# Optimization experiments

Hardware: AMD Instinct MI355X
Metric: run time of the kernel (lower is better)

Reference implementation:

```python
import jax, jax.numpy as jnp
import numpy as np

H = 1024            # hinges
S = 4               # shims
N = H + 2           # nodes
NC = 2 * N          # flattened DOFs
B = 256             # batch of independent chains
L = 1.0             # rest edge length
DT = 0.001          # integration step
GAMMA = 2.0         # damping
N_STEPS = 64        # relaxation steps (truncated scan)


def setup_inputs() -> dict:
    key = jax.random.key(0)
    k1, k2, k3, k4, k5 = jax.random.split(key, 5)
    xs = jnp.arange(N, dtype=jnp.float32) * L
    base = jnp.stack([xs, jnp.zeros(N, jnp.float32)], axis=-1)          # (N,2) straight chain
    noise = 0.01 * jax.random.normal(k1, (B, N, 2), jnp.float32)
    noise = noise.at[:, :2, :].set(0.0)                                  # nodes 0,1 fixed exactly
    pos0 = base[None] + noise                                            # (B,N,2)
    tip_base = base[-1]
    tip_off = jnp.stack([-0.1 * L * H * jax.random.uniform(k2, (B,)),
                         2.0 * jax.random.normal(k3, (B,))], axis=-1)
    tip_pos = (tip_base[None] + tip_off).astype(jnp.float32)             # (B,2) imposed tip
    thetas_ss = 0.3 * jax.random.uniform(k4, (H,), jnp.float32)          # snap-through angles
    buckle_arr = jax.random.randint(k5, (H, S), 0, 2).astype(jnp.int32)  # {0,1} -> maps to {-1,+1}
    return dict(pos0=pos0, tip_pos=tip_pos, thetas_ss=thetas_ss, buckle_arr=buckle_arr,
                k_stiff=jnp.float32(10.0), k_soft=jnp.float32(0.5), k_stretch=jnp.float32(1000.0))


def _free_mask():
    m = np.ones(NC, bool)
    m[:4] = False            # nodes 0,1 fixed (dof_idx = 2*node+comp)
    m[2 * (N - 1):] = False  # tip node imposed
    return jnp.asarray(m)


def _energy(x, thetas_ss, buckle_pm, k_stiff, k_soft, k_stretch):
    """Total potential energy of one chain; x is flattened (NC,)."""
    pos = x.reshape(N, 2)
    v1 = pos[1:-1] - pos[:-2]                 # (H,2) edge into hinge h
    v2 = pos[2:] - pos[1:-1]                  # (H,2) edge out of hinge h
    theta = jnp.arctan2(v1[:, 0] * v2[:, 1] - v1[:, 1] * v2[:, 0],
                        jnp.sum(v1 * v2, -1))               # (H,) CCW hinge angle
    d = pos[1:] - pos[:-1]
    elen = jnp.sqrt(jnp.sum(d * d, -1))                     # (H+1,) edge lengths
    T = theta[:, None]                                      # (H,1)
    TH = thetas_ss[:, None]                                 # (H,1)
    stiff = ((buckle_pm == 1) & (T < TH)) | ((buckle_pm == -1) & (T > -TH))  # (H,S)
    k_rot = jnp.where(stiff, k_stiff, k_soft)
    e_rot = 0.5 * jnp.sum(k_rot * (T - TH) ** 2)
    e_str = 0.5 * jnp.sum(k_stretch * (elen - L) ** 2)
    return e_rot + e_str


def reference(pos0, tip_pos, thetas_ss, buckle_arr, k_stiff, k_soft, k_stretch):
    buckle_pm = 2 * buckle_arr - 1                           # {0,1} -> {-1,+1}
    free = _free_mask()                                      # (NC,) static
    x0 = pos0.reshape(B, NC)
    x0 = x0.at[:, 2 * (N - 1)].set(tip_pos[:, 0]).at[:, 2 * (N - 1) + 1].set(tip_pos[:, 1])
    v0 = jnp.zeros_like(x0)

    grad_e = jax.vmap(jax.grad(
        lambda x: _energy(x, thetas_ss, buckle_pm, k_stiff, k_soft, k_stretch)))

    def step(carry, _):
        x, v = carry
        f = -grad_e(x)                                       # potential force, (B,NC)
        v = jnp.where(free[None], v + DT * (f - GAMMA * v), 0.0)
        x = jnp.where(free[None], x + DT * v, x)             # fixed/imposed DOFs held
        return (x, v), None

    (xf, _vf), _ = jax.lax.scan(step, (x0, v0), None, length=N_STEPS)
    return xf                                                # (B,NC) relaxed positions
```

## Files before the change

### kernel.cpp

```cpp
#include <hip/hip_runtime.h>

#define NN 1026
#define NA 1024
#define BLK 1024

__device__ __forceinline__ float fast_atan2f(float y, float x) {
    float ax = __builtin_fabsf(x), ay = __builtin_fabsf(y);
    float mx = fmaxf(ax, ay), mn = fminf(ax, ay);
    float a  = mn * __builtin_amdgcn_rcpf(mx);
    float s  = a * a;
    float r  = fmaf(s, -0.0117212f,  0.05265332f);
    r = fmaf(s, r, -0.11643287f);
    r = fmaf(s, r,  0.19354346f);
    r = fmaf(s, r, -0.33262347f);
    r = fmaf(s, r,  0.99997726f);
    r *= a;
    if (ay > ax)  r = 1.57079637f - r;
    if (x < 0.0f) r = 3.14159274f - r;
    return copysignf(r, y);
}

__global__ __launch_bounds__(BLK)
void equil_kernel(const float* __restrict__ pos0,
                  const float* __restrict__ tip_pos,
                  const float* __restrict__ thetas_ss,
                  const int*   __restrict__ buckle,
                  const float* __restrict__ kstiff_p,
                  const float* __restrict__ ksoft_p,
                  const float* __restrict__ kstretch_p,
                  float* __restrict__ out)
{
    __shared__ float2 posB0[NN],    posB1[NN];
    __shared__ float2 PsB0[NA + 1], PsB1[NA + 1];
    __shared__ float2 QsB0[NA],     QsB1[NA];

    const int b = blockIdx.x;
    const int t = threadIdx.x;
    const int l = t & 63;
    const float k_str  = kstretch_p[0];
    const float k_sd   = kstiff_p[0] - ksoft_p[0];
    const float k4soft = 4.0f * ksoft_p[0];

    const float2* p0g = (const float2*)(pos0 + (size_t)b * 2052);
    float2 myp;
    if (t < 1023) myp = p0g[t + 2];
    else          { myp.x = tip_pos[2*b]; myp.y = tip_pos[2*b+1]; }
    posB0[t + 2] = myp;  posB1[t + 2] = myp;
    if (t < 2) { posB0[t] = p0g[t]; posB1[t] = p0g[t]; }

    const float TH = thetas_ss[t];
    const int4 bk  = ((const int4*)buckle)[t];
    const float npl = (float)(bk.x + bk.y + bk.z + bk.w);
    float2 vel = make_float2(0.f, 0.f);
    __syncthreads();

#define AB_MATH(posR)                                                         \
        float2 pa = posR[t], pb = posR[t + 1];                                \
        float v1x = pb.x - pa.x,  v1y = pb.y - pa.y;                          \
        float v2x = myp.x - pb.x, v2y = myp.y - pb.y;                         \
        float l2a = fmaf(v1x, v1x, v1y * v1y);                                \
        float l2b = fmaf(v2x, v2x, v2y * v2y);                                \
        float cr  = v1x * v2y - v1y * v2x;                                    \
        float dt_ = fmaf(v1x, v2x, v1y * v2y);                                \
        float theta = fast_atan2f(cr, dt_);                                   \
        float cnt = (theta <  TH ? npl        : 0.f)                          \
                  + (theta > -TH ? 4.f - npl  : 0.f);                         \
        float K = fmaf(cnt, k_sd, k4soft);                                    \
        float m = K * (theta - TH);                                           \
        float ila = __builtin_amdgcn_rsqf(l2a);                               \
        float ilb = __builtin_amdgcn_rsqf(l2b);                               \
        float m1 = m * ila * ila;                                             \
        float m2 = m * ilb * ilb;                                             \
        float2 Bv; Bv.x = -m2 * v2y;  Bv.y =  m2 * v2x;                       \
        float sca = k_str * (1.0f - ila);                                     \
        float2 P;  P.x = fmaf(sca, v1x,  m1 * v1y);                           \
                   P.y = fmaf(sca, v1y, -m1 * v1x);                           \
        float2 Q;  Q.x = P.x - Bv.x;  Q.y = P.y - Bv.y;

    {
        AB_MATH(posB0)
        PsB1[t] = P;
        QsB1[t] = Q;
        if (t == NA - 1) {
            float scb = k_str * (1.0f - ilb);
            PsB1[NA] = make_float2(scb * v2x, scb * v2y);
        }
    }
    __syncthreads();

#define STEP(posR, posW, PsF, QsF, PsS, QsS)                                  \
    {                                                                         \
        AB_MATH(posR)                                                         \
        PsF[t] = P;                                                           \
        QsF[t] = Q;                                                           \
        if (t == NA - 1) {                                                    \
            float scb = k_str * (1.0f - ilb);                                 \
            PsF[NA] = make_float2(scb * v2x, scb * v2y);                      \
        }                                                                     \
        __asm__ __volatile__("" ::: "memory");   \
        if (t < 1023) {                                                       \
            float2 Pn = (l >= 62 ? PsS : PsF)[t + 2];                         \
            float2 Qm = (l == 63 ? QsS : QsF)[t + 1];                         \
            float fx = Pn.x - Qm.x - Bv.x;                                    \
            float fy = Pn.y - Qm.y - Bv.y;                                    \
            vel.x += 0.001f * (fx - 2.0f * vel.x);                            \
            vel.y += 0.001f * (fy - 2.0f * vel.y);                            \
            myp.x += 0.001f * vel.x;                                          \
            myp.y += 0.001f * vel.y;                                          \
            posW[t + 2] = myp;                                                \
        }                                                                     \
        __syncthreads();                                                      \
    }

    for (int s2 = 0; s2 < 32; ++s2) {
        STEP(posB0, posB1, PsB0, QsB0, PsB1, QsB1)
        STEP(posB1, posB0, PsB1, QsB1, PsB0, QsB0)
    }
#undef STEP
#undef AB_MATH

    float2* o = (float2*)(out + (size_t)b * 2052);
    o[t + 2] = myp;
    if (t < 2) o[t] = posB0[t];
}

extern "C" void kernel_launch(void* const* d_in, const int* in_sizes, int n_in,
                              void* d_out, int out_size, void* d_ws, size_t ws_size,
                              hipStream_t stream) {
    const float* pos0   = (const float*)d_in[0];
    const float* tip    = (const float*)d_in[1];
    const float* thetas = (const float*)d_in[2];
    const int*   buckle = (const int*)  d_in[3];
    const float* ks     = (const float*)d_in[4];
    const float* ko     = (const float*)d_in[5];
    const float* kr     = (const float*)d_in[6];
    float* out = (float*)d_out;
    hipLaunchKernelGGL(equil_kernel, dim3(256), dim3(BLK), 0, stream,
                       pos0, tip, thetas, buckle, ks, ko, kr, out);
}
```

Before: 45.12 us.

## Restructure P/Q shared buffers into per-wave rows with halo slots

Replaces the flat P and Q shared arrays with a per-wavefront padded layout (stride 132) where each wave's row carries halo slots. The next wave's first two lanes write their values ahead into the previous wave's halo, so the read no longer has to pick between current and previous buffers per lane. The aim is to remove the divergent buffer-select addressing in the inner step and keep loads contiguous within a row. In exchange, two lanes per wave do extra halo writes and the code depends on careful handling of the halo and boundary slots.

```diff
diff --git a/kernel.cpp b/kernel.cpp
--- a/kernel.cpp
+++ b/kernel.cpp
@@ -3,6 +3,8 @@
 #define NN 1026
 #define NA 1024
 #define BLK 1024
+#define RSTR 132
+#define QOFF 66
 
 __device__ __forceinline__ float fast_atan2f(float y, float x) {
     float ax = __builtin_fabsf(x), ay = __builtin_fabsf(y);
@@ -30,13 +32,15 @@
                   const float* __restrict__ kstretch_p,
                   float* __restrict__ out)
 {
-    __shared__ float2 posB0[NN],    posB1[NN];
-    __shared__ float2 PsB0[NA + 1], PsB1[NA + 1];
-    __shared__ float2 QsB0[NA],     QsB1[NA];
+    __shared__ float2 posA[NN], posB[NN];
+    __shared__ float2 PQ[2][17 * RSTR];
 
     const int b = blockIdx.x;
     const int t = threadIdx.x;
-    const int l = t & 63;
+    const int w = t >> 6, l = t & 63;
+    const int myslot = w * RSTR + l;
+    const int hreg   = (w == 0) ? 16 : w - 1;
+    const int hslot  = hreg * RSTR + 64 + l;
     const float k_str  = kstretch_p[0];
     const float k_sd   = kstiff_p[0] - ksoft_p[0];
     const float k4soft = 4.0f * ksoft_p[0];
@@ -45,8 +49,13 @@
     float2 myp;
     if (t < 1023) myp = p0g[t + 2];
     else          { myp.x = tip_pos[2*b]; myp.y = tip_pos[2*b+1]; }
-    posB0[t + 2] = myp;  posB1[t + 2] = myp;
-    if (t < 2) { posB0[t] = p0g[t]; posB1[t] = p0g[t]; }
+    posA[t + 2] = myp;  posB[t + 2] = myp;
+    if (t < 2) { posA[t] = p0g[t]; posB[t] = p0g[t]; }
+    if (t < 2) {
+        PQ[t][15*RSTR + 65]        = make_float2(0.f, 0.f);
+        PQ[t][15*RSTR + QOFF + 64] = make_float2(0.f, 0.f);
+        PQ[t][15*RSTR + QOFF + 65] = make_float2(0.f, 0.f);
+    }
 
     const float TH = thetas_ss[t];
     const int4 bk  = ((const int4*)buckle)[t];
@@ -78,29 +87,36 @@
         float2 Q;  Q.x = P.x - Bv.x;  Q.y = P.y - Bv.y;
 
     {
-        AB_MATH(posB0)
-        PsB1[t] = P;
-        QsB1[t] = Q;
-        if (t == NA - 1) {
-            float scb = k_str * (1.0f - ilb);
-            PsB1[NA] = make_float2(scb * v2x, scb * v2y);
+        AB_MATH(posA)
+        if (l < 2) {
+            float2* H = &PQ[0][hslot];
+            H[0]    = P;
+            H[QOFF] = Q;
         }
+        (void)Bv;
     }
     __syncthreads();
 
-#define STEP(posR, posW, PsF, QsF, PsS, QsS)                                  \
+#define STEP(posR, posW, CUR, NXT)                                            \
     {                                                                         \
         AB_MATH(posR)                                                         \
-        PsF[t] = P;                                                           \
-        QsF[t] = Q;                                                           \
-        if (t == NA - 1) {                                                    \
+        float2* Wo = &PQ[CUR][myslot];                                        \
+        Wo[0]    = P;                                      \
+        Wo[QOFF] = Q;                                                         \
+        if (l < 2) {                             \
+            float2* H = &PQ[NXT][hslot];                                      \
+            H[0]    = P;                                                      \
+            H[QOFF] = Q;                                                      \
+        }                                                                     \
+        if (t == 1023) {                         \
             float scb = k_str * (1.0f - ilb);                                 \
-            PsF[NA] = make_float2(scb * v2x, scb * v2y);                      \
+            PQ[CUR][15*RSTR + 64] = make_float2(scb * v2x, scb * v2y);        \
         }                                                                     \
-        __asm__ __volatile__("" ::: "memory");   \
+        __asm__ __volatile__("" ::: "memory");                                \
+        const float2* R = &PQ[CUR][myslot];                                   \
+        float2 Pn = R[2];                            \
+        float2 Qm = R[QOFF + 1];                                              \
         if (t < 1023) {                                                       \
-            float2 Pn = (l >= 62 ? PsS : PsF)[t + 2];                         \
-            float2 Qm = (l == 63 ? QsS : QsF)[t + 1];                         \
             float fx = Pn.x - Qm.x - Bv.x;                                    \
             float fy = Pn.y - Qm.y - Bv.y;                                    \
             vel.x += 0.001f * (fx - 2.0f * vel.x);                            \
@@ -113,15 +129,15 @@
     }
 
     for (int s2 = 0; s2 < 32; ++s2) {
-        STEP(posB0, posB1, PsB0, QsB0, PsB1, QsB1)
-        STEP(posB1, posB0, PsB1, QsB1, PsB0, QsB0)
+        STEP(posA, posB, 0, 1)
+        STEP(posB, posA, 1, 0)
     }
 #undef STEP
 #undef AB_MATH
 
     float2* o = (float2*)(out + (size_t)b * 2052);
     o[t + 2] = myp;
-    if (t < 2) o[t] = posB0[t];
+    if (t < 2) o[t] = posA[t];
 }
 
 extern "C" void kernel_launch(void* const* d_in, const int* in_sizes, int n_in,
```

Result: slower. 46.63 us (+3.3%).

## Run two relaxation substeps per block barrier using wave-seam exchange buffers

Applied to the files above, without the earlier changes.

Replaces the per-step block-wide barrier and ping-pong position/force buffers with single shared arrays. Each 64-lane wave reads its own neighbours directly from LDS within the wave. Values crossing wave boundaries are exchanged through small double-buffered seam arrays that are refreshed only every second step, so there is one __syncthreads per two integration steps. This halves barrier cost, but nodes at wave boundaries now use neighbour data that is one step stale, so results drift slightly from the reference dynamics.

```diff
diff --git a/kernel.cpp b/kernel.cpp
--- a/kernel.cpp
+++ b/kernel.cpp
@@ -30,13 +30,16 @@
                   const float* __restrict__ kstretch_p,
                   float* __restrict__ out)
 {
-    __shared__ float2 posB0[NN],    posB1[NN];
-    __shared__ float2 PsB0[NA + 1], PsB1[NA + 1];
-    __shared__ float2 QsB0[NA],     QsB1[NA];
+    __shared__ float2 pos[NN];
+    __shared__ float2 Ps[NA + 2];
+    __shared__ float2 Qs[NA + 1];
+    __shared__ float2 seamPos[2][16][2];
+    __shared__ float2 seamPQ[2][17][3];
 
     const int b = blockIdx.x;
     const int t = threadIdx.x;
-    const int l = t & 63;
+    const int w = t >> 6, l = t & 63;
+    const int pqreg = (w == 0) ? 16 : w - 1;
     const float k_str  = kstretch_p[0];
     const float k_sd   = kstiff_p[0] - ksoft_p[0];
     const float k4soft = 4.0f * ksoft_p[0];
@@ -45,8 +48,8 @@
     float2 myp;
     if (t < 1023) myp = p0g[t + 2];
     else          { myp.x = tip_pos[2*b]; myp.y = tip_pos[2*b+1]; }
-    posB0[t + 2] = myp;  posB1[t + 2] = myp;
-    if (t < 2) { posB0[t] = p0g[t]; posB1[t] = p0g[t]; }
+    pos[t + 2] = myp;
+    if (t < 2) pos[t] = p0g[t];
 
     const float TH = thetas_ss[t];
     const int4 bk  = ((const int4*)buckle)[t];
@@ -54,8 +57,7 @@
     float2 vel = make_float2(0.f, 0.f);
     __syncthreads();
 
-#define AB_MATH(posR)                                                         \
-        float2 pa = posR[t], pb = posR[t + 1];                                \
+#define AB_BODY                                                               \
         float v1x = pb.x - pa.x,  v1y = pb.y - pa.y;                          \
         float v2x = myp.x - pb.x, v2y = myp.y - pb.y;                         \
         float l2a = fmaf(v1x, v1x, v1y * v1y);                                \
@@ -78,50 +80,67 @@
         float2 Q;  Q.x = P.x - Bv.x;  Q.y = P.y - Bv.y;
 
     {
-        AB_MATH(posB0)
-        PsB1[t] = P;
-        QsB1[t] = Q;
-        if (t == NA - 1) {
-            float scb = k_str * (1.0f - ilb);
-            PsB1[NA] = make_float2(scb * v2x, scb * v2y);
+        float2 pa = pos[t], pb = pos[t + 1];
+        AB_BODY
+        (void)Bv; (void)ilb; (void)v2x; (void)v2y;
+        if (l >= 62) seamPos[0][w][l - 62] = myp;
+        if (l < 2) {
+            seamPQ[0][pqreg][l] = P;
+            if (l == 0) seamPQ[0][pqreg][2] = Q;
         }
     }
     __syncthreads();
 
-#define STEP(posR, posW, PsF, QsF, PsS, QsS)                                  \
+#define SUBSTEP(CUR, NXT, DOPUSH)                                             \
     {                                                                         \
-        AB_MATH(posR)                                                         \
-        PsF[t] = P;                                                           \
-        QsF[t] = Q;                                                           \
-        if (t == NA - 1) {                                                    \
+        float2 pa, pb;                                                        \
+        if (w > 0 && l < 2) {                                                 \
+            pa = seamPos[CUR][w - 1][l];                                      \
+            pb = (l == 0) ? seamPos[CUR][w - 1][1] : pos[t + 1];              \
+        } else {                                                              \
+            pa = pos[t];  pb = pos[t + 1];                                    \
+        }                                                                     \
+        AB_BODY                                                               \
+        Ps[t] = P;  Qs[t] = Q;                                                \
+        if (t == NA - 1) {      \
             float scb = k_str * (1.0f - ilb);                                 \
-            PsF[NA] = make_float2(scb * v2x, scb * v2y);                      \
+            Ps[NA] = make_float2(scb * v2x, scb * v2y);                       \
         }                                                                     \
-        __asm__ __volatile__("" ::: "memory");   \
+        __asm__ __volatile__("" ::: "memory");                                \
+        const bool sm = (l >= 62) && (w < 15);                                \
+        float2 Pn = sm ? seamPQ[CUR][w][l - 62] : Ps[t + 2];                  \
+        float2 Qm = (sm && l == 63) ? seamPQ[CUR][w][2] : Qs[t + 1];          \
         if (t < 1023) {                                                       \
-            float2 Pn = (l >= 62 ? PsS : PsF)[t + 2];                         \
-            float2 Qm = (l == 63 ? QsS : QsF)[t + 1];                         \
             float fx = Pn.x - Qm.x - Bv.x;                                    \
             float fy = Pn.y - Qm.y - Bv.y;                                    \
             vel.x += 0.001f * (fx - 2.0f * vel.x);                            \
             vel.y += 0.001f * (fy - 2.0f * vel.y);                            \
             myp.x += 0.001f * vel.x;                                          \
             myp.y += 0.001f * vel.y;                                          \
-            posW[t + 2] = myp;                                                \
+            pos[t + 2] = myp;                                                 \
         }                                                                     \
-        __syncthreads();                                                      \
+        if (DOPUSH) {                                                         \
+            if (l >= 62) seamPos[NXT][w][l - 62] = myp;                       \
+            if (l < 2) {                                                      \
+                seamPQ[NXT][pqreg][l] = P;                                    \
+                if (l == 0) seamPQ[NXT][pqreg][2] = Q;                        \
+            }                                                                 \
+        }                                                                     \
+        __asm__ __volatile__("" ::: "memory");                                \
     }
 
-    for (int s2 = 0; s2 < 32; ++s2) {
-        STEP(posB0, posB1, PsB0, QsB0, PsB1, QsB1)
-        STEP(posB1, posB0, PsB1, QsB1, PsB0, QsB0)
+    for (int blk = 0; blk < 32; ++blk) {
+        const int cur = blk & 1, nxt = cur ^ 1;
+        SUBSTEP(cur, nxt, 0)
+        SUBSTEP(cur, nxt, 1)
+        __syncthreads();
     }
-#undef STEP
-#undef AB_MATH
+#undef SUBSTEP
+#undef AB_BODY
 
     float2* o = (float2*)(out + (size_t)b * 2052);
     o[t + 2] = myp;
-    if (t < 2) o[t] = posB0[t];
+    if (t < 2) o[t] = pos[t];
 }
 
 extern "C" void kernel_launch(void* const* d_in, const int* in_sizes, int n_in,
```

New measurement: 47.36 us. +5.0%, slower.
